# Performance work log

Measured on AMD Instinct MI355X. Metric: run time of the kernel, lower is better.

The kernel has to match this reference:

```python
import jax, jax.numpy as jnp
from jax import lax
import numpy as np
import math

B, N, M, SIG, HID, NFEAT, OUT, H = 256, 512, 16, 256, 256, 3, 10, 256
ALPHA, BETA = 1.0, 0.5


def setup_inputs() -> dict:
    key = jax.random.key(0)
    ks = jax.random.split(key, 12)
    s_g = 1.0 / math.sqrt(HID)
    s_f = 1.0 / math.sqrt(SIG)
    return {
        "x": jax.random.normal(ks[0], (B, 1, H, H), jnp.float32),
        "unif": jax.random.uniform(ks[1], (B, N), jnp.float32),
        "z": jax.random.normal(ks[2], (B, N, 2), jnp.float32),
        "m_g_params": jax.random.normal(ks[3], (1, 6 * M), jnp.float32),
        "gc1_w": jax.random.uniform(ks[4], (NFEAT, HID), jnp.float32, -s_g, s_g),
        "gc1_b": jax.random.uniform(ks[5], (HID,), jnp.float32, -s_g, s_g),
        "gc2_w": jax.random.uniform(ks[6], (HID, HID), jnp.float32, -s_g, s_g),
        "gc2_b": jax.random.uniform(ks[7], (HID,), jnp.float32, -s_g, s_g),
        "collapser1": 0.1 * jax.random.normal(ks[8], (SIG, N), jnp.float32),
        "collapser2": 0.1 * jax.random.normal(ks[9], (SIG, N), jnp.float32),
        "fcf_w": jax.random.uniform(ks[10], (OUT, SIG), jnp.float32, -s_f, s_f),
        "fcf_b": jax.random.uniform(ks[11], (OUT,), jnp.float32, -s_f, s_f),
    }


def _mixture_fields(m_g_params):
    # torch: split [num_sample, 6M] into M chunks of 6, stack -> [M, N, 6],
    # split along last dim, then .view(N, M) in C-order on the [M, N] field.
    raw = m_g_params.reshape(M, 6)  # [M, 6]
    return [jnp.broadcast_to(raw[:, j][:, None], (M, N)).reshape(N, M) for j in range(6)]


def reference(x, unif, z, m_g_params, gc1_w, gc1_b, gc2_w, gc2_b,
              collapser1, collapser2, fcf_w, fcf_b):
    pi_f, mux_f, muy_f, sx_f, sy_f, rho_f = _mixture_fields(m_g_params)
    pi = jax.nn.softmax(pi_f, axis=-1)            # [N, M]
    # categorical sampling via CDF inversion, vectorized over batch
    cdf = jnp.cumsum(pi, axis=-1)                 # [N, M]
    idx = jnp.argmax(unif[:, :, None] < cdf[None], axis=-1)  # [B, N]
    row = jnp.arange(N)[None, :]
    gat = lambda f: f[row, idx]                   # [B, N]
    mux, muy = gat(mux_f), gat(muy_f)
    sx, sy = jnp.exp(gat(sx_f)), jnp.exp(gat(sy_f))
    rho = jnp.tanh(gat(rho_f))
    # reparameterized bivariate-normal sample via Cholesky (lower)
    z1, z2 = z[..., 0], z[..., 1]
    xs = mux + sx * z1
    ys = muy + sy * (rho * z1 + jnp.sqrt(1.0 - rho * rho) * z2)
    # torch MVN.sample() is no_grad -> detach samples
    xs_c, ys_c = lax.stop_gradient(xs), lax.stop_gradient(ys)
    dx, dy = xs_c - mux, ys_c - muy
    omr2 = 1.0 - rho * rho
    quad = (dx * dx / (sx * sx) - 2.0 * rho * dx * dy / (sx * sy) + dy * dy / (sy * sy)) / omr2
    logprob = (-jnp.log(2.0 * jnp.pi) - jnp.log(sx * sy)
               - 0.5 * jnp.log(omr2) - 0.5 * quad)  # [B, N]
    full_log_prob = logprob.sum(axis=-1)           # [B]
    loc = jnp.tanh(jnp.stack([xs_c, ys_c], axis=-1))  # [B, N, 2]
    # adjacency: inverse shifted pairwise squared distance
    diff = loc[:, :, None, :] - loc[:, None, :, :]  # [B, N, N, 2]
    adj = 1.0 / (ALPHA + BETA * jnp.sum(diff * diff, axis=-1))  # [B, N, N]
    # pixel gather: denormalize (trunc toward zero, like torch .long())
    pix = jnp.trunc(0.5 * (loc + 1.0) * H - 0.1).astype(jnp.int32)
    pix = jnp.clip(pix, 0, H - 1)
    bidx = jnp.arange(B)[:, None]
    pv = x[bidx, :, pix[..., 0], pix[..., 1]]      # [B, N, 1]
    feat = jnp.concatenate([pv, loc], axis=-1)     # [B, N, 3]
    # GCN (eval mode: no dropout)
    s1 = jax.nn.relu(jnp.einsum('bnm,bmh->bnh', adj, feat @ gc1_w) + gc1_b)
    s2 = jax.nn.relu(jnp.einsum('bnm,bmh->bnh', adj, s1 @ gc2_w) + gc2_b)
    # nn.Softmax() (no dim) on 3D input resolves to dim=0 in torch
    g1 = jax.nn.softmax(jnp.einsum('sn,bnh->bsh', collapser1, s1), axis=0)
    g2 = jax.nn.softmax(jnp.einsum('sn,bnh->bsh', collapser2, s2), axis=0)
    sig = (g1 + g2).sum(axis=2)                    # [B, SIG]
    out = jax.nn.softmax(sig @ fcf_w.T + fcf_b, axis=-1)  # [B, OUT]
    return out, full_log_prob
```

## Files before the change

### kernel.cpp

```cpp
#include <hip/hip_runtime.h>
#include <hip/hip_bf16.h>
#include <math.h>

#define Bx   256
#define Nx   512
#define SIGx 256
#define HIDx 256
#define OUTx 10
#define Hx   256

typedef __attribute__((ext_vector_type(4))) float f32x4;
typedef __attribute__((ext_vector_type(2))) uint uint2v;
typedef long fp8x8;
typedef unsigned char uchar;

#define WAITVM(N) asm volatile("s_waitcnt vmcnt(" #N ")" ::: "memory")
#define MEMFENCE() asm volatile("" ::: "memory")

__device__ inline uchar f2fp8(float v) {
    int r = __builtin_amdgcn_cvt_pk_fp8_f32(v, 0.0f, 0, false);
    return (uchar)(r & 0xff);
}
__device__ inline uint pk4fp8(float a0, float a1, float a2, float a3) {
    int r = __builtin_amdgcn_cvt_pk_fp8_f32(a0, a1, 0, false);
    r = __builtin_amdgcn_cvt_pk_fp8_f32(a2, a3, r, true);
    return (uint)r;
}

__device__ inline void gload_lds16(const uchar* g, uchar* l) {
    __builtin_amdgcn_global_load_lds(
        (const __attribute__((address_space(1))) uint*)g,
        (__attribute__((address_space(3))) uint*)l, 16, 0, 0);
}
__device__ inline const uchar* laddr(const uchar* base, int row, int kb) {
    int ps = (kb >> 4) ^ ((row >> 1) & 3) ^ ((row >> 4) & 3);
    return base + row*64 + ps*16 + (kb & 15);
}
__device__ inline const uchar* laddrB(const uchar* base, int row, int kb) {
    int ps = ((kb >> 4) & 7) ^ (row & 7);
    return base + row*128 + ps*16 + (kb & 15);
}
__device__ inline int xcd_chunk(int bid, int nwg) {
    return ((nwg & 7) == 0) ? ((bid & 7) * (nwg >> 3) + (bid >> 3)) : bid;
}

__global__ __launch_bounds__(512) void kA_sample(
    const float* __restrict__ x, const float* __restrict__ z,
    const float* __restrict__ mg, float* __restrict__ feat,
    float* __restrict__ flp)
{
    int b = blockIdx.x;
    int n = threadIdx.x;
    int g = n >> 5;
    float mux = mg[g*6+1];
    float muy = mg[g*6+2];
    float sxv = expf(mg[g*6+3]);
    float syv = expf(mg[g*6+4]);
    float rho = tanhf(mg[g*6+5]);
    float z1 = z[((size_t)b*Nx + n)*2 + 0];
    float z2 = z[((size_t)b*Nx + n)*2 + 1];
    float omr2 = 1.0f - rho*rho;
    float xs = mux + sxv*z1;
    float ys = muy + syv*(rho*z1 + sqrtf(omr2)*z2);
    float dx = xs - mux, dy = ys - muy;
    float quad = (dx*dx/(sxv*sxv) - 2.0f*rho*dx*dy/(sxv*syv) + dy*dy/(syv*syv)) / omr2;
    float logprob = -1.8378770664093453f - logf(sxv*syv) - 0.5f*logf(omr2) - 0.5f*quad;
    float lx = tanhf(xs), ly = tanhf(ys);
    int px = (int)truncf(0.5f*(lx+1.0f)*(float)Hx - 0.1f);
    int py = (int)truncf(0.5f*(ly+1.0f)*(float)Hx - 0.1f);
    px = px < 0 ? 0 : (px > Hx-1 ? Hx-1 : px);
    py = py < 0 ? 0 : (py > Hx-1 ? Hx-1 : py);
    float pv = x[(size_t)b*Hx*Hx + (size_t)px*Hx + py];
    size_t fo = ((size_t)b*Nx + n)*3;
    feat[fo+0] = pv; feat[fo+1] = lx; feat[fo+2] = ly;

    __shared__ float red[512];
    red[n] = logprob;
    __syncthreads();
    for (int st = 256; st > 0; st >>= 1) {
        if (n < st) red[n] += red[n+st];
        __syncthreads();
    }
    if (n == 0) flp[b] = red[0];
}

__global__ __launch_bounds__(256) void kPrep(
    const float* __restrict__ c1, const float* __restrict__ c2,
    const float* __restrict__ w2,
    uchar* __restrict__ c1q, uchar* __restrict__ c2q, uchar* __restrict__ w2tq)
{
    int idx = blockIdx.x*256 + threadIdx.x;
    if (idx < SIGx*Nx) {
        c1q[idx] = f2fp8(16.0f * c1[idx]);
        c2q[idx] = f2fp8(16.0f * c2[idx]);
    }
    if (idx < HIDx*HIDx) {
        int i = idx >> 8, j = idx & 255;
        w2tq[idx] = f2fp8(16.0f * w2[j*HIDx + i]);
    }
}

__global__ __launch_bounds__(512) void kFuse1S(
    const float* __restrict__ featL, const float* __restrict__ w1,
    const float* __restrict__ b1,
    uchar* __restrict__ adjAll, uchar* __restrict__ s1tAll)
{
    int b = blockIdx.x;
    int n0 = blockIdx.y * 256;
    const float* fb = featL + (size_t)b*Nx*3;
    uchar* adj = adjAll + (size_t)b*Nx*Nx;
    uchar* s1t = s1tAll + (size_t)b*HIDx*Nx;

    __shared__ float fpv[Nx], flx[Nx], fly[Nx], fH[Nx];
    __shared__ float w1s[3*HIDx], b1s[HIDx];
    __shared__ float Gp[8][3][256];

    int t = threadIdx.x;
    {
        float pv = fb[t*3+0], lx = fb[t*3+1], ly = fb[t*3+2];
        fpv[t] = pv; flx[t] = lx; fly[t] = ly;
        fH[t] = fmaf(0.5f*lx, lx, fmaf(0.5f*ly, ly, 1.0f));
    }
    for (int i = t; i < 3*HIDx; i += 512) w1s[i] = w1[i];
    if (t < HIDx) b1s[t] = b1[t];
    __syncthreads();

    int tq = t & 63;
    int mc = t >> 6;
    int lc = tq*4;
    int n4 = n0 + lc;

    float xn[4], yn[4], cn[4];
    #pragma unroll
    for (int e = 0; e < 4; ++e) {
        xn[e] = flx[n4+e]; yn[e] = fly[n4+e];
        cn[e] = fmaf(0.5f*xn[e], xn[e], 0.5f*yn[e]*yn[e]);
    }
    float G0[4] = {}, G1[4] = {}, G2[4] = {};

    int m0 = mc*64;
    #pragma unroll 4
    for (int mm = 0; mm < 64; ++mm) {
        int m = m0 + mm;
        float hx = fH[m], fx = flx[m], fy = fly[m];
        float a[4];
        #pragma unroll
        for (int e = 0; e < 4; ++e) {
            float s = fmaf(-yn[e], fy, fmaf(-xn[e], fx, hx + cn[e]));
            a[e] = __builtin_amdgcn_rcpf(s);
            G0[e] = fmaf(a[e], fpv[m], G0[e]);
            G1[e] = fmaf(a[e], fx, G1[e]);
            G2[e] = fmaf(a[e], fy, G2[e]);
        }
        *(uint*)(adj + (size_t)m*Nx + n4) = pk4fp8(a[0], a[1], a[2], a[3]);
    }

    *(f32x4*)&Gp[mc][0][lc] = (f32x4){G0[0],G0[1],G0[2],G0[3]};
    *(f32x4*)&Gp[mc][1][lc] = (f32x4){G1[0],G1[1],G1[2],G1[3]};
    *(f32x4*)&Gp[mc][2][lc] = (f32x4){G2[0],G2[1],G2[2],G2[3]};
    __syncthreads();

    f32x4 T0 = {}, T1 = {}, T2 = {};
    #pragma unroll
    for (int j = 0; j < 8; ++j) {
        T0 += *(const f32x4*)&Gp[j][0][lc];
        T1 += *(const f32x4*)&Gp[j][1][lc];
        T2 += *(const f32x4*)&Gp[j][2][lc];
    }

    int hc = mc;
    #pragma unroll 4
    for (int hh = 0; hh < 32; ++hh) {
        int h = hc*32 + hh;
        float w0 = w1s[h], wA = w1s[HIDx+h], wB = w1s[2*HIDx+h], bb = b1s[h];
        float v0 = fminf(fmaxf(fmaf(T0.x,w0, fmaf(T1.x,wA, fmaf(T2.x,wB, bb))), 0.0f), 448.0f);
        float v1 = fminf(fmaxf(fmaf(T0.y,w0, fmaf(T1.y,wA, fmaf(T2.y,wB, bb))), 0.0f), 448.0f);
        float v2 = fminf(fmaxf(fmaf(T0.z,w0, fmaf(T1.z,wA, fmaf(T2.z,wB, bb))), 0.0f), 448.0f);
        float v3 = fminf(fmaxf(fmaf(T0.w,w0, fmaf(T1.w,wA, fmaf(T2.w,wB, bb))), 0.0f), 448.0f);
        *(uint*)(s1t + (size_t)h*Nx + n4) = pk4fp8(v0, v1, v2, v3);
    }
}

__global__ __launch_bounds__(512, 4) void kGemmAdjB(
    const uchar* __restrict__ Aall, const uchar* __restrict__ adjAll,
    const float* __restrict__ bias, uchar* __restrict__ outAll)
{
    int w = xcd_chunk(blockIdx.x, gridDim.x);
    int b    = w >> 3;
    int tile = w & 7;
    int rt = tile >> 2;
    int ct = tile & 3;
    const uchar* A = Aall + (size_t)b*HIDx*Nx;
    const uchar* Badj = adjAll + (size_t)b*Nx*Nx;
    uchar* outp = outAll + (size_t)b*HIDx*Nx;

    __shared__ __align__(16) uchar Als[2][128*128];
    __shared__ __align__(16) uchar Bls[2][128*128];
    int t = threadIdx.x;
    int lane = t & 63, wave = t >> 6;
    int wr = wave >> 2, wc = wave & 3;
    int q = lane >> 4, c16 = lane & 15;
    int r0 = rt*128, n0 = ct*128;
    int srow0 = t >> 3;
    int su0   = t & 7;
    f32x4 acc[4][2] = {};

    auto stage = [&](int buf, int kkv) {
        #pragma unroll
        for (int p = 0; p < 2; ++p) {
            int row = p*64 + srow0;
            int su = su0 ^ (row & 7);
            gload_lds16(A + (size_t)(r0+row)*Nx + kkv + su*16,
                        Als[buf] + p*8192 + wave*1024);
            gload_lds16(Badj + (size_t)(n0+row)*Nx + kkv + su*16,
                        Bls[buf] + p*8192 + wave*1024);
        }
    };

    const int nt = Nx/128;
    stage(0, 0);
    for (int i = 0; i < nt; ++i) {
        if (i < nt-1) { stage((i+1)&1, (i+1)*128); WAITVM(4); }
        else WAITVM(0);
        __builtin_amdgcn_s_barrier();
        MEMFENCE();
        const uchar* Ac = Als[i&1];
        const uchar* Bc = Bls[i&1];
        #pragma unroll
        for (int ks = 0; ks < 128; ks += 32) {
            fp8x8 af[4], bfr[2];
            #pragma unroll
            for (int i2 = 0; i2 < 4; ++i2)
                af[i2] = *(const fp8x8*)laddrB(Ac, wr*64 + i2*16 + c16, ks + q*8);
            #pragma unroll
            for (int j = 0; j < 2; ++j)
                bfr[j] = *(const fp8x8*)laddrB(Bc, wc*32 + j*16 + c16, ks + q*8);
            #pragma unroll
            for (int i2 = 0; i2 < 4; ++i2)
                #pragma unroll
                for (int j = 0; j < 2; ++j)
                    acc[i2][j] = __builtin_amdgcn_mfma_f32_16x16x32_fp8_fp8(af[i2], bfr[j], acc[i2][j], 0, 0, 0);
        }
        MEMFENCE();
        __builtin_amdgcn_s_barrier();
        MEMFENCE();
    }
    #pragma unroll
    for (int i = 0; i < 4; ++i) {
        int rowb = r0 + wr*64 + i*16 + q*4;
        #pragma unroll
        for (int j = 0; j < 2; ++j) {
            int col = n0 + wc*32 + j*16 + c16;
            #pragma unroll
            for (int r = 0; r < 4; ++r) {
                float v = fmaxf(acc[i][j][r] + bias[rowb + r], 0.0f) * 0.25f;
                outp[(size_t)(rowb + r)*Nx + col] = f2fp8(fminf(v, 448.0f));
            }
        }
    }
}

__global__ __launch_bounds__(512, 4) void kGstd8(
    const uchar* __restrict__ Ash, const uchar* __restrict__ Ball,
    uchar* __restrict__ outAll, float oscale)
{
    int w = xcd_chunk(blockIdx.x, gridDim.x);
    int b    = w >> 2;
    int tile = w & 3;
    int rt = tile >> 1;
    int ct = tile & 1;
    const uchar* B = Ball + (size_t)b*HIDx*Nx;
    uchar* outp = outAll + (size_t)b*HIDx*256;

    __shared__ __align__(16) uchar Als[2][128*64];
    __shared__ __align__(16) uchar Bls[2][128*64];
    int t = threadIdx.x;
    int lane = t & 63, wave = t >> 6;
    int wr = wave >> 2, wc = wave & 3;
    int q = lane >> 4, c16 = lane & 15;
    int r0 = rt*128, n0 = ct*128;
    int srow = wave*16 + (lane >> 2);
    int pu   = lane & 3;
    int sl   = pu ^ ((srow>>1)&3) ^ ((srow>>4)&3);
    f32x4 acc[4][2] = {};

    auto stage = [&](int buf, int kkv) {
        gload_lds16(Ash + (size_t)(r0+srow)*Nx + kkv + sl*16, Als[buf] + wave*1024);
        gload_lds16(B + (size_t)(n0+srow)*Nx + kkv + sl*16, Bls[buf] + wave*1024);
    };

    const int nt = Nx/64;
    stage(0, 0);
    for (int i = 0; i < nt; ++i) {
        if (i < nt-1) { stage((i+1)&1, (i+1)*64); WAITVM(2); }
        else WAITVM(0);
        __builtin_amdgcn_s_barrier();
        MEMFENCE();
        const uchar* Ac = Als[i&1];
        const uchar* Bc = Bls[i&1];
        #pragma unroll
        for (int ks = 0; ks < 64; ks += 32) {
            fp8x8 af[4], bfr[2];
            #pragma unroll
            for (int i2 = 0; i2 < 4; ++i2)
                af[i2] = *(const fp8x8*)laddr(Ac, wr*64 + i2*16 + c16, ks + q*8);
            #pragma unroll
            for (int j = 0; j < 2; ++j)
                bfr[j] = *(const fp8x8*)laddr(Bc, wc*32 + j*16 + c16, ks + q*8);
            #pragma unroll
            for (int i2 = 0; i2 < 4; ++i2)
                #pragma unroll
                for (int j = 0; j < 2; ++j)
                    acc[i2][j] = __builtin_amdgcn_mfma_f32_16x16x32_fp8_fp8(af[i2], bfr[j], acc[i2][j], 0, 0, 0);
        }
        MEMFENCE();
        __builtin_amdgcn_s_barrier();
        MEMFENCE();
    }
    #pragma unroll
    for (int i = 0; i < 4; ++i) {
        int rowb = r0 + wr*64 + i*16 + q*4;
        #pragma unroll
        for (int j = 0; j < 2; ++j) {
            int col = n0 + wc*32 + j*16 + c16;
            #pragma unroll
            for (int r = 0; r < 4; ++r) {
                float v = acc[i][j][r] * oscale;
                v = fminf(fmaxf(v, -448.0f), 448.0f);
                outp[(size_t)(rowb + r)*256 + col] = f2fp8(v);
            }
        }
    }
}

__global__ __launch_bounds__(512, 4) void kGstdT8(
    const uchar* __restrict__ Ash, const uchar* __restrict__ Ball,
    uchar* __restrict__ outAll, float oscale)
{
    const int K = 256, NC = 512;
    int w = xcd_chunk(blockIdx.x, gridDim.x);
    int b    = w >> 3;
    int tile = w & 7;
    int rt = tile >> 2;
    int ct = tile & 3;
    const uchar* B = Ball + (size_t)b*HIDx*Nx;
    uchar* outp = outAll + (size_t)b*HIDx*NC;

    __shared__ __align__(16) uchar Als[2][128*64];
    __shared__ __align__(16) uchar Bls[2][128*64];
    int t = threadIdx.x;
    int lane = t & 63, wave = t >> 6;
    int wr = wave >> 2, wc = wave & 3;
    int q = lane >> 4, c16 = lane & 15;
    int r0 = rt*128, n0 = ct*128;
    int srow = wave*16 + (lane >> 2);
    int pu   = lane & 3;
    int sl   = pu ^ ((srow>>1)&3) ^ ((srow>>4)&3);
    int pi  = t & 31;
    int g   = t >> 5;
    int nc8 = g & 7;
    int ch  = g >> 3;
    f32x4 acc[4][2] = {};

    auto stageA = [&](int buf, int kkv) {
        gload_lds16(Ash + (size_t)(r0+srow)*K + kkv + sl*16, Als[buf] + wave*1024);
    };
    auto loadBT = [&](int kkv, uint2v& v0, uint2v& v1) {
        int hk = kkv + 2*pi;
        const uchar* g0 = B + (size_t)hk*NC + n0 + nc8*16 + ch*8;
        v0 = *(const uint2v*)g0;
        v1 = *(const uint2v*)(g0 + NC);
    };
    auto writeBT = [&](int buf, const uint2v& v0, const uint2v& v1) {
        const uchar* pa = (const uchar*)&v0;
        const uchar* qa = (const uchar*)&v1;
        int kb = 2*pi;
        int s  = kb >> 4;
        #pragma unroll
        for (int e = 0; e < 8; ++e) {
            int row = nc8*16 + ch*8 + e;
            int ps = s ^ ((row>>1)&3) ^ ((row>>4)&3);
            *(ushort*)(Bls[buf] + row*64 + ps*16 + (kb & 15)) =
                (ushort)pa[e] | ((ushort)qa[e] << 8);
        }
    };
    auto mfmaStep = [&](int buf) {
        const uchar* Ac = Als[buf];
        const uchar* Bc = Bls[buf];
        #pragma unroll
        for (int ks = 0; ks < 64; ks += 32) {
            fp8x8 af[4], bfr[2];
            #pragma unroll
            for (int i = 0; i < 4; ++i)
                af[i] = *(const fp8x8*)laddr(Ac, wr*64 + i*16 + c16, ks + q*8);
            #pragma unroll
            for (int j = 0; j < 2; ++j)
                bfr[j] = *(const fp8x8*)laddr(Bc, wc*32 + j*16 + c16, ks + q*8);
            #pragma unroll
            for (int i = 0; i < 4; ++i)
                #pragma unroll
                for (int j = 0; j < 2; ++j)
                    acc[i][j] = __builtin_amdgcn_mfma_f32_16x16x32_fp8_fp8(af[i], bfr[j], acc[i][j], 0, 0, 0);
        }
    };

    uint2v bv0, bv1;
    stageA(0, 0);
    loadBT(0, bv0, bv1); writeBT(0, bv0, bv1);
    __syncthreads();
    for (int kk = 0; kk < K; kk += 64) {
        int cur = (kk >> 6) & 1, nxt = cur ^ 1;
        bool more = (kk + 64) < K;
        if (more) {
            stageA(nxt, kk + 64);
            loadBT(kk + 64, bv0, bv1);
        }
        mfmaStep(cur);
        if (more) writeBT(nxt, bv0, bv1);
        __syncthreads();
    }
    #pragma unroll
    for (int i = 0; i < 4; ++i) {
        int rowb = r0 + wr*64 + i*16 + q*4;
        #pragma unroll
        for (int j = 0; j < 2; ++j) {
            int col = n0 + wc*32 + j*16 + c16;
            #pragma unroll
            for (int r = 0; r < 4; ++r) {
                float v = acc[i][j][r] * oscale;
                v = fminf(fmaxf(v, -448.0f), 448.0f);
                outp[(size_t)(rowb + r)*NC + col] = f2fp8(v);
            }
        }
    }
}

__global__ __launch_bounds__(512) void kF1q(
    const uchar* __restrict__ t1, const uchar* __restrict__ t2,
    float* __restrict__ m1, float* __restrict__ rd1,
    float* __restrict__ m2, float* __restrict__ rd2)
{
    int s = blockIdx.x;
    int t = threadIdx.x;
    int hq = t & 63;
    int bq = t >> 6;
    const size_t str = (size_t)SIGx*HIDx;
    size_t base = (size_t)(bq*32)*str + (size_t)s*HIDx + hq*4;

    float mv1[4], dv1[4], mv2[4], dv2[4];
    #pragma unroll
    for (int e = 0; e < 4; ++e) { mv1[e]=-3.0e38f; dv1[e]=0.0f; mv2[e]=-3.0e38f; dv2[e]=0.0f; }

    for (int i = 0; i < 32; ++i) {
        uint u1 = *(const uint*)(t1 + base + (size_t)i*str);
        uint u2 = *(const uint*)(t2 + base + (size_t)i*str);
        float v1[4], v2[4];
        v1[0] = __builtin_amdgcn_cvt_f32_fp8(u1, 0);
        v1[1] = __builtin_amdgcn_cvt_f32_fp8(u1, 1);
        v1[2] = __builtin_amdgcn_cvt_f32_fp8(u1, 2);
        v1[3] = __builtin_amdgcn_cvt_f32_fp8(u1, 3);
        v2[0] = __builtin_amdgcn_cvt_f32_fp8(u2, 0);
        v2[1] = __builtin_amdgcn_cvt_f32_fp8(u2, 1);
        v2[2] = __builtin_amdgcn_cvt_f32_fp8(u2, 2);
        v2[3] = __builtin_amdgcn_cvt_f32_fp8(u2, 3);
        #pragma unroll
        for (int e = 0; e < 4; ++e) {
            float mn;
            mn = fmaxf(mv1[e], v1[e]);
            dv1[e] = dv1[e]*__expf(mv1[e]-mn) + __expf(v1[e]-mn); mv1[e] = mn;
            mn = fmaxf(mv2[e], v2[e]);
            dv2[e] = dv2[e]*__expf(mv2[e]-mn) + __expf(v2[e]-mn); mv2[e] = mn;
        }
    }

    __shared__ float pm1[8][256], pd1[8][256], pm2[8][256], pd2[8][256];
    #pragma unroll
    for (int e = 0; e < 4; ++e) {
        pm1[bq][hq*4+e] = mv1[e]; pd1[bq][hq*4+e] = dv1[e];
        pm2[bq][hq*4+e] = mv2[e]; pd2[bq][hq*4+e] = dv2[e];
    }
    __syncthreads();

    if (t < 256) {
        int h = t;
        float m = -3.0e38f, d = 0.0f;
        #pragma unroll
        for (int j = 0; j < 8; ++j) {
            float mm = pm1[j][h], dd = pd1[j][h];
            float mn = fmaxf(m, mm);
            d = d*__expf(m-mn) + dd*__expf(mm-mn);
            m = mn;
        }
        size_t o = (size_t)s*HIDx + h;
        m1[o] = m; rd1[o] = 1.0f/d;
    } else {
        int h = t - 256;
        float m = -3.0e38f, d = 0.0f;
        #pragma unroll
        for (int j = 0; j < 8; ++j) {
            float mm = pm2[j][h], dd = pd2[j][h];
            float mn = fmaxf(m, mm);
            d = d*__expf(m-mn) + dd*__expf(mm-mn);
            m = mn;
        }
        size_t o = (size_t)s*HIDx + h;
        m2[o] = m; rd2[o] = 1.0f/d;
    }
}

__global__ __launch_bounds__(256) void kF2q(
    const uchar* __restrict__ t1, const uchar* __restrict__ t2,
    const float* __restrict__ m1, const float* __restrict__ rd1,
    const float* __restrict__ m2, const float* __restrict__ rd2,
    float* __restrict__ sig)
{
    int b = blockIdx.y;
    int sq = threadIdx.x >> 6;
    int s = blockIdx.x*4 + sq;
    int hq = threadIdx.x & 63;
    size_t sh = (size_t)s*HIDx + hq*4;
    size_t tb = ((size_t)b*SIGx + s)*HIDx + hq*4;
    uint u1 = *(const uint*)(t1 + tb);
    uint u2 = *(const uint*)(t2 + tb);
    f32x4 a1 = *(const f32x4*)&m1[sh];
    f32x4 r1 = *(const f32x4*)&rd1[sh];
    f32x4 a2 = *(const f32x4*)&m2[sh];
    f32x4 r2 = *(const f32x4*)&rd2[sh];
    float v = 0.0f;
    v += __expf(__builtin_amdgcn_cvt_f32_fp8(u1,0) - a1.x) * r1.x;
    v += __expf(__builtin_amdgcn_cvt_f32_fp8(u1,1) - a1.y) * r1.y;
    v += __expf(__builtin_amdgcn_cvt_f32_fp8(u1,2) - a1.z) * r1.z;
    v += __expf(__builtin_amdgcn_cvt_f32_fp8(u1,3) - a1.w) * r1.w;
    v += __expf(__builtin_amdgcn_cvt_f32_fp8(u2,0) - a2.x) * r2.x;
    v += __expf(__builtin_amdgcn_cvt_f32_fp8(u2,1) - a2.y) * r2.y;
    v += __expf(__builtin_amdgcn_cvt_f32_fp8(u2,2) - a2.z) * r2.z;
    v += __expf(__builtin_amdgcn_cvt_f32_fp8(u2,3) - a2.w) * r2.w;

    __shared__ float red[256];
    red[threadIdx.x] = v;
    __syncthreads();
    for (int st = 32; st > 0; st >>= 1) {
        if (hq < st) red[threadIdx.x] += red[threadIdx.x + st];
        __syncthreads();
    }
    if (hq == 0) sig[(size_t)b*SIGx + s] = red[sq*64];
}

__global__ __launch_bounds__(256) void kG_out(
    const float* __restrict__ sig, const float* __restrict__ fw,
    const float* __restrict__ fb, float* __restrict__ out)
{
    int b = blockIdx.x;
    int tid = threadIdx.x;
    __shared__ float red[OUTx][257];
    float sv = sig[(size_t)b*SIGx + tid];
    #pragma unroll
    for (int o = 0; o < OUTx; ++o)
        red[o][tid] = sv * fw[o*SIGx + tid];
    __syncthreads();
    for (int st = 128; st > 0; st >>= 1) {
        if (tid < st) {
            #pragma unroll
            for (int o = 0; o < OUTx; ++o)
                red[o][tid] += red[o][tid + st];
        }
        __syncthreads();
    }
    if (tid == 0) {
        float logits[OUTx];
        float mx = -3.0e38f;
        #pragma unroll
        for (int o = 0; o < OUTx; ++o) {
            logits[o] = red[o][0] + fb[o];
            mx = fmaxf(mx, logits[o]);
        }
        float dd = 0.0f; float e[OUTx];
        #pragma unroll
        for (int o = 0; o < OUTx; ++o) { e[o] = expf(logits[o]-mx); dd += e[o]; }
        float inv = 1.0f/dd;
        #pragma unroll
        for (int o = 0; o < OUTx; ++o) out[(size_t)b*OUTx + o] = e[o]*inv;
    }
}

static inline size_t alignup(size_t b) { return (b + 255) & ~(size_t)255; }

extern "C" void kernel_launch(void* const* d_in, const int* in_sizes, int n_in,
                              void* d_out, int out_size, void* d_ws, size_t ws_size,
                              hipStream_t stream)
{
    const float* x   = (const float*)d_in[0];
    const float* z   = (const float*)d_in[2];
    const float* mg  = (const float*)d_in[3];
    const float* w1  = (const float*)d_in[4];
    const float* b1  = (const float*)d_in[5];
    const float* w2  = (const float*)d_in[6];
    const float* b2  = (const float*)d_in[7];
    const float* c1  = (const float*)d_in[8];
    const float* c2  = (const float*)d_in[9];
    const float* fw  = (const float*)d_in[10];
    const float* fbv = (const float*)d_in[11];
    float* out = (float*)d_out;
    float* flp = out + (size_t)Bx*OUTx;
    (void)in_sizes; (void)n_in; (void)out_size;

    char* ws = (char*)d_ws;
    size_t off = 0;
    auto alloc = [&](size_t bytes) -> char* {
        char* p = ws + off; off += alignup(bytes); return p;
    };
    float*  feat = (float*)alloc((size_t)Bx*Nx*3*4);
    uchar*  c1q  = (uchar*)alloc((size_t)SIGx*Nx);
    uchar*  c2q  = (uchar*)alloc((size_t)SIGx*Nx);
    uchar*  w2tq = (uchar*)alloc((size_t)HIDx*HIDx);
    uchar*  t1   = (uchar*)alloc((size_t)Bx*SIGx*HIDx);
    uchar*  t2   = (uchar*)alloc((size_t)Bx*SIGx*HIDx);
    float*  m1   = (float*)alloc((size_t)SIGx*HIDx*4);
    float*  d1   = (float*)alloc((size_t)SIGx*HIDx*4);
    float*  m2   = (float*)alloc((size_t)SIGx*HIDx*4);
    float*  d2   = (float*)alloc((size_t)SIGx*HIDx*4);
    float*  sig  = (float*)alloc((size_t)Bx*SIGx*4);
    size_t fixed = off;

    int BC = 1;
    for (int c = Bx; c >= 1; c >>= 1) {
        size_t need = fixed + alignup((size_t)c*Nx*Nx)
                            + 2*alignup((size_t)c*HIDx*Nx);
        if (need <= ws_size) { BC = c; break; }
    }
    uchar* Padj = (uchar*)alloc((size_t)BC*Nx*Nx);
    uchar* P1   = (uchar*)alloc((size_t)BC*HIDx*Nx);
    uchar* P2   = (uchar*)alloc((size_t)BC*HIDx*Nx);

    hipLaunchKernelGGL(kA_sample, dim3(Bx), dim3(Nx), 0, stream, x, z, mg, feat, flp);
    hipLaunchKernelGGL(kPrep, dim3(512), dim3(256), 0, stream, c1, c2, w2, c1q, c2q, w2tq);

    const int nch = Bx / BC;
    for (int c = 0; c < nch; ++c) {
        int b0 = c * BC;
        const float* featL = feat + (size_t)b0*Nx*3;
        uchar* t1L = t1 + (size_t)b0*SIGx*HIDx;
        uchar* t2L = t2 + (size_t)b0*SIGx*HIDx;
        hipLaunchKernelGGL(kFuse1S, dim3(BC, 2), dim3(512), 0, stream,
                           featL, w1, b1, Padj, P2);
        hipLaunchKernelGGL(kGstd8, dim3(BC*4), dim3(512), 0, stream,
                           c1q, P2, t1L, 0.0625f);
        hipLaunchKernelGGL(kGstdT8, dim3(BC*8), dim3(512), 0, stream,
                           w2tq, P2, P1, 0.0625f);
        hipLaunchKernelGGL(kGemmAdjB, dim3(BC*8), dim3(512), 0, stream,
                           P1, Padj, b2, P2);
        hipLaunchKernelGGL(kGstd8, dim3(BC*4), dim3(512), 0, stream,
                           c2q, P2, t2L, 0.25f);
    }

    hipLaunchKernelGGL(kF1q, dim3(SIGx), dim3(512), 0, stream,
                       t1, t2, m1, d1, m2, d2);
    hipLaunchKernelGGL(kF2q, dim3(SIGx/4, Bx), dim3(256), 0, stream,
                       t1, t2, m1, d1, m2, d2, sig);
    hipLaunchKernelGGL(kG_out, dim3(Bx), dim3(256), 0, stream, sig, fw, fbv, out);
}
```

Measured before the change: 279.7 us.

## Merge the two P2-consuming GEMMs into one launch and fuse final reductions

The collapser1 GEMM (t1) and the W2 transform GEMM (h2) both read the same s1 activation. They are now issued as one kernel, with blocks split 4/8 by index, replacing two back-to-back launches and letting both tile sets run at the same time. The second-stage softmax-sum and output-layer kernels are fused into one per-batch kernel that reduces with wavefront shuffles and keeps sig in shared memory, which drops the intermediate global buffer and one launch. The fused tail kernel has only 256 blocks, each doing a serial loop of 32 iterations, so it has less parallelism than the earlier 16K-block grid.

```diff
diff --git a/kernel.cpp b/kernel.cpp
--- a/kernel.cpp
+++ b/kernel.cpp
@@ -333,18 +333,15 @@
     }
 }
 
-__global__ __launch_bounds__(512, 4) void kGstdT8(
-    const uchar* __restrict__ Ash, const uchar* __restrict__ Ball,
-    uchar* __restrict__ outAll, float oscale)
-{
-    const int K = 256, NC = 512;
+__global__ __launch_bounds__(512, 4) void kGstdDual(
+    const uchar* __restrict__ c1q, const uchar* __restrict__ w2tq,
+    const uchar* __restrict__ s1tAll,
+    uchar* __restrict__ t1All, uchar* __restrict__ h2All)
+{
     int w = xcd_chunk(blockIdx.x, gridDim.x);
-    int b    = w >> 3;
-    int tile = w & 7;
-    int rt = tile >> 2;
-    int ct = tile & 3;
-    const uchar* B = Ball + (size_t)b*HIDx*Nx;
-    uchar* outp = outAll + (size_t)b*HIDx*NC;
+    int b = w / 12;
+    int j = w % 12;
+    const uchar* B = s1tAll + (size_t)b*HIDx*Nx;
 
     __shared__ __align__(16) uchar Als[2][128*64];
     __shared__ __align__(16) uchar Bls[2][128*64];
@@ -352,38 +349,8 @@
     int lane = t & 63, wave = t >> 6;
     int wr = wave >> 2, wc = wave & 3;
     int q = lane >> 4, c16 = lane & 15;
-    int r0 = rt*128, n0 = ct*128;
-    int srow = wave*16 + (lane >> 2);
-    int pu   = lane & 3;
-    int sl   = pu ^ ((srow>>1)&3) ^ ((srow>>4)&3);
-    int pi  = t & 31;
-    int g   = t >> 5;
-    int nc8 = g & 7;
-    int ch  = g >> 3;
     f32x4 acc[4][2] = {};
 
-    auto stageA = [&](int buf, int kkv) {
-        gload_lds16(Ash + (size_t)(r0+srow)*K + kkv + sl*16, Als[buf] + wave*1024);
-    };
-    auto loadBT = [&](int kkv, uint2v& v0, uint2v& v1) {
-        int hk = kkv + 2*pi;
-        const uchar* g0 = B + (size_t)hk*NC + n0 + nc8*16 + ch*8;
-        v0 = *(const uint2v*)g0;
-        v1 = *(const uint2v*)(g0 + NC);
-    };
-    auto writeBT = [&](int buf, const uint2v& v0, const uint2v& v1) {
-        const uchar* pa = (const uchar*)&v0;
-        const uchar* qa = (const uchar*)&v1;
-        int kb = 2*pi;
-        int s  = kb >> 4;
-        #pragma unroll
-        for (int e = 0; e < 8; ++e) {
-            int row = nc8*16 + ch*8 + e;
-            int ps = s ^ ((row>>1)&3) ^ ((row>>4)&3);
-            *(ushort*)(Bls[buf] + row*64 + ps*16 + (kb & 15)) =
-                (ushort)pa[e] | ((ushort)qa[e] << 8);
-        }
-    };
     auto mfmaStep = [&](int buf) {
         const uchar* Ac = Als[buf];
         const uchar* Bc = Bls[buf];
@@ -394,42 +361,119 @@
             for (int i = 0; i < 4; ++i)
                 af[i] = *(const fp8x8*)laddr(Ac, wr*64 + i*16 + c16, ks + q*8);
             #pragma unroll
-            for (int j = 0; j < 2; ++j)
-                bfr[j] = *(const fp8x8*)laddr(Bc, wc*32 + j*16 + c16, ks + q*8);
+            for (int jj = 0; jj < 2; ++jj)
+                bfr[jj] = *(const fp8x8*)laddr(Bc, wc*32 + jj*16 + c16, ks + q*8);
             #pragma unroll
             for (int i = 0; i < 4; ++i)
                 #pragma unroll
-                for (int j = 0; j < 2; ++j)
-                    acc[i][j] = __builtin_amdgcn_mfma_f32_16x16x32_fp8_fp8(af[i], bfr[j], acc[i][j], 0, 0, 0);
+                for (int jj = 0; jj < 2; ++jj)
+                    acc[i][jj] = __builtin_amdgcn_mfma_f32_16x16x32_fp8_fp8(af[i], bfr[jj], acc[i][jj], 0, 0, 0);
         }
     };
 
-    uint2v bv0, bv1;
-    stageA(0, 0);
-    loadBT(0, bv0, bv1); writeBT(0, bv0, bv1);
-    __syncthreads();
-    for (int kk = 0; kk < K; kk += 64) {
-        int cur = (kk >> 6) & 1, nxt = cur ^ 1;
-        bool more = (kk + 64) < K;
-        if (more) {
-            stageA(nxt, kk + 64);
-            loadBT(kk + 64, bv0, bv1);
-        }
-        mfmaStep(cur);
-        if (more) writeBT(nxt, bv0, bv1);
+    if (j < 4) {
+        int rt = j >> 1, ct = j & 1;
+        int r0 = rt*128, n0 = ct*128;
+        uchar* outp = t1All + (size_t)b*SIGx*HIDx;
+        int srow = wave*16 + (lane >> 2);
+        int pu   = lane & 3;
+        int sl   = pu ^ ((srow>>1)&3) ^ ((srow>>4)&3);
+
+        auto stage = [&](int buf, int kkv) {
+            gload_lds16(c1q + (size_t)(r0+srow)*Nx + kkv + sl*16, Als[buf] + wave*1024);
+            gload_lds16(B + (size_t)(n0+srow)*Nx + kkv + sl*16, Bls[buf] + wave*1024);
+        };
+        const int nt = Nx/64;
+        stage(0, 0);
+        for (int i = 0; i < nt; ++i) {
+            if (i < nt-1) { stage((i+1)&1, (i+1)*64); WAITVM(2); }
+            else WAITVM(0);
+            __builtin_amdgcn_s_barrier();
+            MEMFENCE();
+            mfmaStep(i&1);
+            MEMFENCE();
+            __builtin_amdgcn_s_barrier();
+            MEMFENCE();
+        }
+        #pragma unroll
+        for (int i = 0; i < 4; ++i) {
+            int rowb = r0 + wr*64 + i*16 + q*4;
+            #pragma unroll
+            for (int jj = 0; jj < 2; ++jj) {
+                int col = n0 + wc*32 + jj*16 + c16;
+                #pragma unroll
+                for (int r = 0; r < 4; ++r) {
+                    float v = acc[i][jj][r] * 0.0625f;
+                    v = fminf(fmaxf(v, -448.0f), 448.0f);
+                    outp[(size_t)(rowb + r)*HIDx + col] = f2fp8(v);
+                }
+            }
+        }
+    } else {
+        const int K = 256, NC = 512;
+        int tile = j - 4;
+        int rt = tile >> 2;
+        int ct = tile & 3;
+        int r0 = rt*128, n0 = ct*128;
+        uchar* outp = h2All + (size_t)b*HIDx*NC;
+        int srow = wave*16 + (lane >> 2);
+        int pu   = lane & 3;
+        int sl   = pu ^ ((srow>>1)&3) ^ ((srow>>4)&3);
+        int pi  = t & 31;
+        int g   = t >> 5;
+        int nc8 = g & 7;
+        int ch  = g >> 3;
+
+        auto stageA = [&](int buf, int kkv) {
+            gload_lds16(w2tq + (size_t)(r0+srow)*K + kkv + sl*16, Als[buf] + wave*1024);
+        };
+        auto loadBT = [&](int kkv, uint2v& v0, uint2v& v1) {
+            int hk = kkv + 2*pi;
+            const uchar* g0 = B + (size_t)hk*NC + n0 + nc8*16 + ch*8;
+            v0 = *(const uint2v*)g0;
+            v1 = *(const uint2v*)(g0 + NC);
+        };
+        auto writeBT = [&](int buf, const uint2v& v0, const uint2v& v1) {
+            const uchar* pa = (const uchar*)&v0;
+            const uchar* qa = (const uchar*)&v1;
+            int kb = 2*pi;
+            int s  = kb >> 4;
+            #pragma unroll
+            for (int e = 0; e < 8; ++e) {
+                int row = nc8*16 + ch*8 + e;
+                int ps = s ^ ((row>>1)&3) ^ ((row>>4)&3);
+                *(ushort*)(Bls[buf] + row*64 + ps*16 + (kb & 15)) =
+                    (ushort)pa[e] | ((ushort)qa[e] << 8);
+            }
+        };
+
+        uint2v bv0, bv1;
+        stageA(0, 0);
+        loadBT(0, bv0, bv1); writeBT(0, bv0, bv1);
         __syncthreads();
-    }
-    #pragma unroll
-    for (int i = 0; i < 4; ++i) {
-        int rowb = r0 + wr*64 + i*16 + q*4;
-        #pragma unroll
-        for (int j = 0; j < 2; ++j) {
-            int col = n0 + wc*32 + j*16 + c16;
-            #pragma unroll
-            for (int r = 0; r < 4; ++r) {
-                float v = acc[i][j][r] * oscale;
-                v = fminf(fmaxf(v, -448.0f), 448.0f);
-                outp[(size_t)(rowb + r)*NC + col] = f2fp8(v);
+        for (int kk = 0; kk < K; kk += 64) {
+            int cur = (kk >> 6) & 1, nxt = cur ^ 1;
+            bool more = (kk + 64) < K;
+            if (more) {
+                stageA(nxt, kk + 64);
+                loadBT(kk + 64, bv0, bv1);
+            }
+            mfmaStep(cur);
+            if (more) writeBT(nxt, bv0, bv1);
+            __syncthreads();
+        }
+        #pragma unroll
+        for (int i = 0; i < 4; ++i) {
+            int rowb = r0 + wr*64 + i*16 + q*4;
+            #pragma unroll
+            for (int jj = 0; jj < 2; ++jj) {
+                int col = n0 + wc*32 + jj*16 + c16;
+                #pragma unroll
+                for (int r = 0; r < 4; ++r) {
+                    float v = acc[i][jj][r] * 0.0625f;
+                    v = fminf(fmaxf(v, -448.0f), 448.0f);
+                    outp[(size_t)(rowb + r)*NC + col] = f2fp8(v);
+                }
             }
         }
     }
@@ -508,65 +552,62 @@
     }
 }
 
-__global__ __launch_bounds__(256) void kF2q(
+__global__ __launch_bounds__(512) void kFG(
     const uchar* __restrict__ t1, const uchar* __restrict__ t2,
     const float* __restrict__ m1, const float* __restrict__ rd1,
     const float* __restrict__ m2, const float* __restrict__ rd2,
-    float* __restrict__ sig)
-{
-    int b = blockIdx.y;
-    int sq = threadIdx.x >> 6;
-    int s = blockIdx.x*4 + sq;
-    int hq = threadIdx.x & 63;
-    size_t sh = (size_t)s*HIDx + hq*4;
-    size_t tb = ((size_t)b*SIGx + s)*HIDx + hq*4;
-    uint u1 = *(const uint*)(t1 + tb);
-    uint u2 = *(const uint*)(t2 + tb);
-    f32x4 a1 = *(const f32x4*)&m1[sh];
-    f32x4 r1 = *(const f32x4*)&rd1[sh];
-    f32x4 a2 = *(const f32x4*)&m2[sh];
-    f32x4 r2 = *(const f32x4*)&rd2[sh];
-    float v = 0.0f;
-    v += __expf(__builtin_amdgcn_cvt_f32_fp8(u1,0) - a1.x) * r1.x;
-    v += __expf(__builtin_amdgcn_cvt_f32_fp8(u1,1) - a1.y) * r1.y;
-    v += __expf(__builtin_amdgcn_cvt_f32_fp8(u1,2) - a1.z) * r1.z;
-    v += __expf(__builtin_amdgcn_cvt_f32_fp8(u1,3) - a1.w) * r1.w;
-    v += __expf(__builtin_amdgcn_cvt_f32_fp8(u2,0) - a2.x) * r2.x;
-    v += __expf(__builtin_amdgcn_cvt_f32_fp8(u2,1) - a2.y) * r2.y;
-    v += __expf(__builtin_amdgcn_cvt_f32_fp8(u2,2) - a2.z) * r2.z;
-    v += __expf(__builtin_amdgcn_cvt_f32_fp8(u2,3) - a2.w) * r2.w;
-
-    __shared__ float red[256];
-    red[threadIdx.x] = v;
+    const float* __restrict__ fw, const float* __restrict__ fb,
+    float* __restrict__ out)
+{
+    int b = blockIdx.x;
+    int t = threadIdx.x;
+    int sg = t >> 6;
+    int hq = t & 63;
+    __shared__ float sigs[SIGx];
+    __shared__ float red[OUTx][257];
+
+    for (int i = 0; i < 32; ++i) {
+        int s = sg*32 + i;
+        size_t sh = (size_t)s*HIDx + hq*4;
+        size_t tb = ((size_t)b*SIGx + s)*HIDx + hq*4;
+        uint u1 = *(const uint*)(t1 + tb);
+        uint u2 = *(const uint*)(t2 + tb);
+        f32x4 a1 = *(const f32x4*)&m1[sh];
+        f32x4 r1 = *(const f32x4*)&rd1[sh];
+        f32x4 a2 = *(const f32x4*)&m2[sh];
+        f32x4 r2 = *(const f32x4*)&rd2[sh];
+        float v = 0.0f;
+        v += __expf(__builtin_amdgcn_cvt_f32_fp8(u1,0) - a1.x) * r1.x;
+        v += __expf(__builtin_amdgcn_cvt_f32_fp8(u1,1) - a1.y) * r1.y;
+        v += __expf(__builtin_amdgcn_cvt_f32_fp8(u1,2) - a1.z) * r1.z;
+        v += __expf(__builtin_amdgcn_cvt_f32_fp8(u1,3) - a1.w) * r1.w;
+        v += __expf(__builtin_amdgcn_cvt_f32_fp8(u2,0) - a2.x) * r2.x;
+        v += __expf(__builtin_amdgcn_cvt_f32_fp8(u2,1) - a2.y) * r2.y;
+        v += __expf(__builtin_amdgcn_cvt_f32_fp8(u2,2) - a2.z) * r2.z;
+        v += __expf(__builtin_amdgcn_cvt_f32_fp8(u2,3) - a2.w) * r2.w;
+        #pragma unroll
+        for (int msk = 32; msk > 0; msk >>= 1)
+            v += __shfl_xor(v, msk, 64);
+        if (hq == 0) sigs[s] = v;
+    }
     __syncthreads();
-    for (int st = 32; st > 0; st >>= 1) {
-        if (hq < st) red[threadIdx.x] += red[threadIdx.x + st];
-        __syncthreads();
-    }
-    if (hq == 0) sig[(size_t)b*SIGx + s] = red[sq*64];
-}
-
-__global__ __launch_bounds__(256) void kG_out(
-    const float* __restrict__ sig, const float* __restrict__ fw,
-    const float* __restrict__ fb, float* __restrict__ out)
-{
-    int b = blockIdx.x;
-    int tid = threadIdx.x;
-    __shared__ float red[OUTx][257];
-    float sv = sig[(size_t)b*SIGx + tid];
-    #pragma unroll
-    for (int o = 0; o < OUTx; ++o)
-        red[o][tid] = sv * fw[o*SIGx + tid];
+
+    if (t < 256) {
+        float sv = sigs[t];
+        #pragma unroll
+        for (int o = 0; o < OUTx; ++o)
+            red[o][t] = sv * fw[o*SIGx + t];
+    }
     __syncthreads();
     for (int st = 128; st > 0; st >>= 1) {
-        if (tid < st) {
+        if (t < st) {
             #pragma unroll
             for (int o = 0; o < OUTx; ++o)
-                red[o][tid] += red[o][tid + st];
+                red[o][t] += red[o][t + st];
         }
         __syncthreads();
     }
-    if (tid == 0) {
+    if (t == 0) {
         float logits[OUTx];
         float mx = -3.0e38f;
         #pragma unroll
@@ -619,7 +660,6 @@
     float*  d1   = (float*)alloc((size_t)SIGx*HIDx*4);
     float*  m2   = (float*)alloc((size_t)SIGx*HIDx*4);
     float*  d2   = (float*)alloc((size_t)SIGx*HIDx*4);
-    float*  sig  = (float*)alloc((size_t)Bx*SIGx*4);
     size_t fixed = off;
 
     int BC = 1;
@@ -643,10 +683,8 @@
         uchar* t2L = t2 + (size_t)b0*SIGx*HIDx;
         hipLaunchKernelGGL(kFuse1S, dim3(BC, 2), dim3(512), 0, stream,
                            featL, w1, b1, Padj, P2);
-        hipLaunchKernelGGL(kGstd8, dim3(BC*4), dim3(512), 0, stream,
-                           c1q, P2, t1L, 0.0625f);
-        hipLaunchKernelGGL(kGstdT8, dim3(BC*8), dim3(512), 0, stream,
-                           w2tq, P2, P1, 0.0625f);
+        hipLaunchKernelGGL(kGstdDual, dim3(BC*12), dim3(512), 0, stream,
+                           c1q, w2tq, P2, t1L, P1);
         hipLaunchKernelGGL(kGemmAdjB, dim3(BC*8), dim3(512), 0, stream,
                            P1, Padj, b2, P2);
         hipLaunchKernelGGL(kGstd8, dim3(BC*4), dim3(512), 0, stream,
@@ -655,7 +693,6 @@
 
     hipLaunchKernelGGL(kF1q, dim3(SIGx), dim3(512), 0, stream,
                        t1, t2, m1, d1, m2, d2);
-    hipLaunchKernelGGL(kF2q, dim3(SIGx/4, Bx), dim3(256), 0, stream,
-                       t1, t2, m1, d1, m2, d2, sig);
-    hipLaunchKernelGGL(kG_out, dim3(Bx), dim3(256), 0, stream, sig, fw, fbv, out);
-}
+    hipLaunchKernelGGL(kFG, dim3(Bx), dim3(512), 0, stream,
+                       t1, t2, m1, d1, m2, d2, fw, fbv, out);
+}
```

New measurement: 281.9 us. No clear change (+0.8%).
